# Optimization experiments

Hardware: AMD Instinct MI355X
Metric: run time of the kernel (lower is better)

The kernel has to match this reference:

```python
import jax, jax.numpy as jnp
import numpy as np

B, RNN, WV, VOCAB, SRC, NMEM, OOV = 64, 512, 512, 50000, 512, 512, 50


def _gru_cell(x, h, wih, whh, bih, bhh):
    # PyTorch GRU cell. x,h: (B,RNN); wih,whh: (3*RNN, RNN)
    gi = x @ wih.T + bih
    gh = h @ whh.T + bhh
    i_r, i_z, i_n = jnp.split(gi, 3, axis=-1)
    h_r, h_z, h_n = jnp.split(gh, 3, axis=-1)
    r = jax.nn.sigmoid(i_r + h_r)
    z = jax.nn.sigmoid(i_z + h_z)
    n = jnp.tanh(i_n + r * h_n)
    return (1.0 - z) * n + z * h


def _attn_general(q, K, V, mask, W):
    # q: (B,1,D), K/V: (B,N,D), mask: (B,N), W: (D,D) (torch Linear weight, out x in)
    e = jnp.einsum('bnd,ed->bne', K, W)          # W(K)
    e = e * mask[:, :, None]
    en = jnp.einsum('btd,bnd->btn', q, e)        # (B,1,N)
    en = en * mask[:, None, :]
    # masked softmax: exp * mask, renormalize
    m = mask[:, None, :]
    ex = jnp.exp(en - jnp.max(en, axis=-1, keepdims=True)) * m
    w = ex / (jnp.sum(ex, axis=-1, keepdims=True) + 1e-10)
    ctx = jnp.einsum('btn,bnd->btd', w, V)       # (B,1,D)
    return ctx, w, en


def setup_inputs() -> dict:
    key = jax.random.key(0)
    ks = jax.random.split(key, 24)
    s = 0.05
    inp = {
        'y_t_1': jax.random.randint(ks[0], (B,), 0, VOCAB),
        's_t_1': jax.random.normal(ks[1], (1, B, RNN)) * s,
        'encoder_outputs': jax.random.normal(ks[2], (B, SRC, RNN)) * s,
        'enc_padding_mask': jnp.ones((B, SRC), jnp.float32),
        'c_t_1': jax.random.normal(ks[3], (B, 1, RNN)) * s,
        'extra_zeros': jnp.zeros((B, OOV), jnp.float32),
        'enc_batch_extend_vocab': jax.random.randint(ks[4], (B, SRC), 0, VOCAB + OOV),
        'query_memory': jax.random.normal(ks[5], (B, NMEM, RNN)) * s,
        'query_mask': jnp.ones((B, NMEM), jnp.float32),
        # parameters
        'embedding': jax.random.normal(ks[6], (VOCAB, WV)) * s,
        'x_ctx_w': jax.random.normal(ks[7], (RNN, RNN + WV)) * s,
        'x_ctx_b': jnp.zeros((RNN,), jnp.float32),
        'gru_wih': jax.random.uniform(ks[8], (3 * RNN, RNN), minval=-0.1, maxval=0.1),
        'gru_whh': jax.random.uniform(ks[9], (3 * RNN, RNN), minval=-0.1, maxval=0.1),
        'gru_bih': jnp.concatenate([jnp.zeros(RNN), jnp.ones(RNN // 2), jnp.zeros(3 * RNN - RNN - RNN // 2)]).astype(jnp.float32),
        'gru_bhh': jnp.zeros((3 * RNN,), jnp.float32),
        'readq_w': jax.random.normal(ks[10], (RNN, RNN)) * s,
        'readsrc_w': jax.random.normal(ks[11], (RNN, RNN)) * s,
        'out1_w': jax.random.normal(ks[12], (RNN, 2 * RNN)) * s,
        'out1_b': jnp.zeros((RNN,), jnp.float32),
        'out2_w': jax.random.normal(ks[13], (VOCAB, RNN)) * s,
        'out2_b': jnp.zeros((VOCAB,), jnp.float32),
    }
    return inp


def reference(y_t_1, s_t_1, encoder_outputs, enc_padding_mask, c_t_1, extra_zeros,
              enc_batch_extend_vocab, query_memory, query_mask,
              embedding, x_ctx_w, x_ctx_b, gru_wih, gru_whh, gru_bih, gru_bhh,
              readq_w, readsrc_w, out1_w, out1_b, out2_w, out2_b):
    # embed current token and mix with previous context
    y_emb = embedding[y_t_1]                                   # (B,WV)
    x = jnp.concatenate([c_t_1, y_emb[:, None, :]], axis=-1)   # (B,1,RNN+WV)
    x = x @ x_ctx_w.T + x_ctx_b                                # (B,1,RNN)

    h = s_t_1[0]                                               # (B,RNN)
    h = _gru_cell(x[:, 0], h, gru_wih, gru_whh, gru_bih, gru_bhh)

    # NTM memory read + second GRU step (loop runs once in the source)
    c_mem, _, _ = _attn_general(h[:, None, :], query_memory, query_memory, query_mask, readq_w)
    h = _gru_cell(c_mem[:, 0], h, gru_wih, gru_whh, gru_bih, gru_bhh)

    # source attention
    c_t, attn_dist, _ = _attn_general(h[:, None, :], encoder_outputs, encoder_outputs, enc_padding_mask, readsrc_w)

    out = jnp.concatenate([h, c_t[:, 0]], axis=-1)             # (B,2*RNN)
    out = out @ out1_w.T + out1_b
    out = out @ out2_w.T + out2_b                              # (B,VOCAB)
    vocab_dist = jax.nn.softmax(out, axis=-1)

    vocab_dist_ = 0.5 * vocab_dist
    attn_dist_ = 0.5 * attn_dist[:, 0]                         # (B,SRC)
    vocab_dist_ = jnp.concatenate([vocab_dist_, extra_zeros], axis=-1)  # (B,VOCAB+OOV)

    # copy-mechanism scatter_add along vocab dim, per batch row
    final_dist = jax.vmap(lambda v, idx, a: v.at[idx].add(a))(
        vocab_dist_, enc_batch_extend_vocab, attn_dist_)

    s_t = h[None]                                              # (1,B,RNN)
    return final_dist, s_t, c_t, attn_dist
```

## Files before the change

### kernel.cpp

```cpp
#include <hip/hip_runtime.h>

#define BATCH 64
#define RNN   512
#define VOCAB 50000
#define OOV   50
#define VEXT  50050
#define NSRC  512

typedef short bf16x8 __attribute__((ext_vector_type(8)));
typedef float f32x4  __attribute__((ext_vector_type(4)));

__device__ __forceinline__ float sigmoidf_(float x) { return 1.f / (1.f + __expf(-x)); }

__device__ __forceinline__ short f2bf(float x) {
    unsigned u = __builtin_bit_cast(unsigned, x);
    unsigned r = (u + 0x7FFFu + ((u >> 16) & 1u)) >> 16;
    return (short)r;
}

__global__ void k_build_x0(const int* __restrict__ y, const float* __restrict__ c_t_1,
                           const float* __restrict__ emb, float* __restrict__ x0)
{
    const int b = blockIdx.x;
    const int row = y[b];
    for (int d = threadIdx.x; d < 512; d += 256) {
        x0[(size_t)b * 1024 + d]       = c_t_1[(size_t)b * 512 + d];
        x0[(size_t)b * 1024 + 512 + d] = emb[(size_t)row * 512 + d];
    }
}

template<bool WT>
__global__ __launch_bounds__(256) void k_gemm_small(
    const float* __restrict__ A0, const float* __restrict__ W0,
    const float* __restrict__ bias0, float* __restrict__ C0, int asum0,
    const float* __restrict__ A1, const float* __restrict__ W1,
    const float* __restrict__ bias1, float* __restrict__ C1, int asum1,
    int K, int O)
{
    const float* A = A0; const float* W = W0; const float* bias = bias0;
    float* C = C0; int asum = asum0;
    if (blockIdx.z == 1) { A = A1; W = W1; bias = bias1; C = C1; asum = asum1; }

    __shared__ float As[32 * 64];
    __shared__ float Ws[32 * 32];
    const int t  = threadIdx.x;
    const int tx = t & 15, ty = t >> 4;
    const int o0 = blockIdx.x * 32;
    const int kchunk = K >> 2;
    const int kbeg = blockIdx.y * kchunk;
    const int kend = kbeg + kchunk;
    float acc[4][2] = {};
    const int ab  = t >> 2;
    const int akq = (t & 3) * 4;

    for (int k0 = kbeg; k0 < kend; k0 += 32) {
        {
            const float* Ap = &A[(size_t)ab * K + k0 + akq];
            float4 v0 = *(const float4*)Ap;
            float4 v1 = *(const float4*)(Ap + 16);
            if (asum) {
                #pragma unroll
                for (int s = 1; s < 4; s++) {
                    const float* Aps = Ap + (size_t)s * 64 * K;
                    float4 w0 = *(const float4*)Aps;
                    float4 w1 = *(const float4*)(Aps + 16);
                    v0.x += w0.x; v0.y += w0.y; v0.z += w0.z; v0.w += w0.w;
                    v1.x += w1.x; v1.y += w1.y; v1.z += w1.z; v1.w += w1.w;
                }
            }
            As[(akq+0)*64+ab]=v0.x; As[(akq+1)*64+ab]=v0.y; As[(akq+2)*64+ab]=v0.z; As[(akq+3)*64+ab]=v0.w;
            As[(akq+16)*64+ab]=v1.x; As[(akq+17)*64+ab]=v1.y; As[(akq+18)*64+ab]=v1.z; As[(akq+19)*64+ab]=v1.w;
        }
        if (WT) {
            const int o  = t >> 3;
            const int kq = (t & 7) * 4;
            float4 v = *(const float4*)&W[(size_t)(o0 + o) * K + k0 + kq];
            Ws[(kq+0)*32+o]=v.x; Ws[(kq+1)*32+o]=v.y; Ws[(kq+2)*32+o]=v.z; Ws[(kq+3)*32+o]=v.w;
        } else {
            const int kk = t >> 3;
            const int oq = (t & 7) * 4;
            *(float4*)&Ws[kk*32 + oq] = *(const float4*)&W[(size_t)(k0 + kk) * O + o0 + oq];
        }
        __syncthreads();
        #pragma unroll
        for (int kk = 0; kk < 32; kk++) {
            float4 a4 = *(const float4*)&As[kk*64 + ty*4];
            float2 w2 = *(const float2*)&Ws[kk*32 + tx*2];
            acc[0][0] = fmaf(a4.x, w2.x, acc[0][0]); acc[0][1] = fmaf(a4.x, w2.y, acc[0][1]);
            acc[1][0] = fmaf(a4.y, w2.x, acc[1][0]); acc[1][1] = fmaf(a4.y, w2.y, acc[1][1]);
            acc[2][0] = fmaf(a4.z, w2.x, acc[2][0]); acc[2][1] = fmaf(a4.z, w2.y, acc[2][1]);
            acc[3][0] = fmaf(a4.w, w2.x, acc[3][0]); acc[3][1] = fmaf(a4.w, w2.y, acc[3][1]);
        }
        __syncthreads();
    }
    const int o = o0 + tx*2;
    float b0v = 0.f, b1v = 0.f;
    if (bias && blockIdx.y == 0) { b0v = bias[o]; b1v = bias[o+1]; }
    float* Cp = C + (size_t)blockIdx.y * 64 * O;
    #pragma unroll
    for (int j = 0; j < 4; j++) {
        const int bb = ty*4 + j;
        Cp[(size_t)bb*O + o]     = acc[j][0] + b0v;
        Cp[(size_t)bb*O + o + 1] = acc[j][1] + b1v;
    }
}

__global__ void k_gru_elem(const float* __restrict__ gi, const float* __restrict__ gh,
                           const float* __restrict__ h, float* __restrict__ hout,
                           float* __restrict__ cat_out)
{
    const int b = blockIdx.x, d = threadIdx.x;
    float ir = 0, iz = 0, inn = 0, hr = 0, hz = 0, hn = 0;
    #pragma unroll
    for (int s = 0; s < 4; s++) {
        const float* gis = gi + (size_t)s * BATCH * 1536 + (size_t)b * 1536;
        const float* ghs = gh + (size_t)s * BATCH * 1536 + (size_t)b * 1536;
        ir += gis[d]; iz += gis[512 + d]; inn += gis[1024 + d];
        hr += ghs[d]; hz += ghs[512 + d]; hn += ghs[1024 + d];
    }
    const float r = sigmoidf_(ir + hr);
    const float z = sigmoidf_(iz + hz);
    const float n = tanhf(inn + r * hn);
    const float hv = (1.f - z) * n + z * h[(size_t)b * 512 + d];
    hout[(size_t)b * 512 + d] = hv;
    if (cat_out) cat_out[(size_t)b * 1024 + d] = hv;
}

__global__ __launch_bounds__(256) void k_attn_pass(
    const float* __restrict__ KV, const float* __restrict__ Upart,
    const float* __restrict__ mask, float* __restrict__ en, float* __restrict__ part)
{
    const int b = blockIdx.y;
    const int chunk = blockIdx.x;
    const int t = threadIdx.x;
    const int lane = t & 63;
    const int wv = t >> 6;
    const float* KVb = KV + (size_t)b * NSRC * RNN;

    const int r0 = chunk * 32 + wv * 8;

    float4 x[8][2];
    float mk[8];
    #pragma unroll
    for (int i = 0; i < 8; i++) {
        const float* rp = KVb + (size_t)(r0 + i) * RNN + lane * 8;
        x[i][0] = *(const float4*)rp;
        x[i][1] = *(const float4*)(rp + 4);
    }
    #pragma unroll
    for (int i = 0; i < 8; i++) mk[i] = mask[(size_t)b * NSRC + r0 + i];

    float4 u0, u1;
    {
        const float* up = Upart + (size_t)b * RNN + lane * 8;
        u0 = *(const float4*)up; u1 = *(const float4*)(up + 4);
        #pragma unroll
        for (int s = 1; s < 4; s++) {
            const float* ups = up + (size_t)s * BATCH * RNN;
            float4 a = *(const float4*)ups; float4 c = *(const float4*)(ups + 4);
            u0.x += a.x; u0.y += a.y; u0.z += a.z; u0.w += a.w;
            u1.x += c.x; u1.y += c.y; u1.z += c.z; u1.w += c.w;
        }
    }

    float m_run = -1e30f, s_run = 0.f;
    float acc[8] = {0,0,0,0,0,0,0,0};
    #pragma unroll
    for (int i = 0; i < 8; i++) {
        const int n = r0 + i;
        float d = x[i][0].x*u0.x + x[i][0].y*u0.y + x[i][0].z*u0.z + x[i][0].w*u0.w
                + x[i][1].x*u1.x + x[i][1].y*u1.y + x[i][1].z*u1.z + x[i][1].w*u1.w;
        #pragma unroll
        for (int off = 32; off; off >>= 1) d += __shfl_xor(d, off);
        const float s = d * mk[i] * mk[i];
        if (lane == 0) en[(size_t)b * NSRC + n] = s;
        const float mnew = fmaxf(m_run, s);
        const float sc = __expf(m_run - mnew);
        const float w  = __expf(s - mnew) * mk[i];
        s_run = s_run * sc + w;
        acc[0] = acc[0]*sc + w*x[i][0].x; acc[1] = acc[1]*sc + w*x[i][0].y;
        acc[2] = acc[2]*sc + w*x[i][0].z; acc[3] = acc[3]*sc + w*x[i][0].w;
        acc[4] = acc[4]*sc + w*x[i][1].x; acc[5] = acc[5]*sc + w*x[i][1].y;
        acc[6] = acc[6]*sc + w*x[i][1].z; acc[7] = acc[7]*sc + w*x[i][1].w;
        m_run = mnew;
    }
    __shared__ float sm[4], ss[4];
    __shared__ float sacc[4][512];
    *(float4*)&sacc[wv][lane*8]     = make_float4(acc[0], acc[1], acc[2], acc[3]);
    *(float4*)&sacc[wv][lane*8 + 4] = make_float4(acc[4], acc[5], acc[6], acc[7]);
    if (lane == 0) { sm[wv] = m_run; ss[wv] = s_run; }
    __syncthreads();
    const float M = fmaxf(fmaxf(sm[0], sm[1]), fmaxf(sm[2], sm[3]));
    const float e0 = __expf(sm[0]-M), e1 = __expf(sm[1]-M), e2 = __expf(sm[2]-M), e3 = __expf(sm[3]-M);
    const float S = ss[0]*e0 + ss[1]*e1 + ss[2]*e2 + ss[3]*e3;
    float* pp = part + (size_t)(b * 16 + chunk) * 514;
    const int c = t;
    pp[2 + c]       = sacc[0][c]*e0 + sacc[1][c]*e1 + sacc[2][c]*e2 + sacc[3][c]*e3;
    pp[2 + c + 256] = sacc[0][c+256]*e0 + sacc[1][c+256]*e1 + sacc[2][c+256]*e2 + sacc[3][c+256]*e3;
    if (t == 0) { pp[0] = M; pp[1] = S; }
}

__global__ __launch_bounds__(256) void k_attn_combine(
    const float* __restrict__ part, const float* __restrict__ en,
    const float* __restrict__ mask, float* __restrict__ ctx,
    float* __restrict__ ctx2, float* __restrict__ attn_out)
{
    const int b = blockIdx.x, t = threadIdx.x;
    const float* pb = part + (size_t)b * 16 * 514;
    float M = -1e30f;
    #pragma unroll
    for (int c = 0; c < 16; c++) M = fmaxf(M, pb[c * 514]);
    float e[16]; float S = 0.f;
    #pragma unroll
    for (int c = 0; c < 16; c++) { e[c] = __expf(pb[c * 514] - M); S += pb[c * 514 + 1] * e[c]; }
    const float inv = 1.f / (S + 1e-10f);
    for (int d = t; d < 512; d += 256) {
        float a = 0.f;
        #pragma unroll
        for (int c = 0; c < 16; c++) a += pb[c * 514 + 2 + d] * e[c];
        const float val = a * inv;
        ctx[(size_t)b * 512 + d] = val;
        if (ctx2) ctx2[(size_t)b * 1024 + d] = val;
    }
    if (attn_out) {
        for (int n = t; n < NSRC; n += 256)
            attn_out[(size_t)b * NSRC + n] = __expf(en[(size_t)b * NSRC + n] - M) * mask[(size_t)b * NSRC + n] * inv;
    }
}

__global__ void k_tobf16(const float* __restrict__ in, short* __restrict__ outp)
{
    const int i = blockIdx.x * 256 + threadIdx.x;
    const float v = in[i] + in[32768 + i] + in[65536 + i] + in[98304 + i];
    outp[i] = f2bf(v);
}

__global__ __launch_bounds__(512, 4) void k_out2_mfma(
    const short* __restrict__ Abf, const float* __restrict__ W2,
    const float* __restrict__ bias, float* __restrict__ C)
{
    __shared__ alignas(16) short As[64 * 512];
    const int t = threadIdx.x;
    const int lane = t & 63, wv = t >> 6;

    {
        char* Asb = (char*)As;
        const char* Ab = (const char*)Abf;
        #pragma unroll
        for (int it = 0; it < 8; ++it) {
            const int off = (it * 512 + t) * 16;
            const int row = off >> 10;
            const int kb  = off & 1023;
            bf16x8 v = *(const bf16x8*)(Ab + off);
            *(bf16x8*)(Asb + row * 1024 + (kb ^ ((row & 7) << 4))) = v;
        }
    }
    __syncthreads();

    const int l15 = lane & 15, g = lane >> 4;
    const int goff = g * 8;
    const int obase = blockIdx.x * 128 + wv * 16;
    const int ocol = obase + l15;
    const int orow = (ocol < VOCAB) ? ocol : (VOCAB - 1);
    const float* wr = &W2[(size_t)orow * RNN + goff];

    const int sw = (l15 & 7) << 4;
    const char* a0b = (const char*)As + (l15     ) * 1024;
    const char* a1b = (const char*)As + (l15 + 16) * 1024;
    const char* a2b = (const char*)As + (l15 + 32) * 1024;
    const char* a3b = (const char*)As + (l15 + 48) * 1024;

    f32x4 acc0 = {0,0,0,0}, acc1 = {0,0,0,0}, acc2 = {0,0,0,0}, acc3 = {0,0,0,0};

    float4 p0a = *(const float4*)(wr);
    float4 p0b = *(const float4*)(wr + 4);
    float4 p1a = *(const float4*)(wr + 32);
    float4 p1b = *(const float4*)(wr + 36);
    #pragma unroll 4
    for (int k0 = 0; k0 < RNN; k0 += 32) {
        const int kn = (k0 + 64) & 511;
        float4 n0 = *(const float4*)(wr + kn);
        float4 n1 = *(const float4*)(wr + kn + 4);
        const int kb = ((k0 + goff) * 2) ^ sw;
        bf16x8 a0 = *(const bf16x8*)(a0b + kb);
        bf16x8 a1 = *(const bf16x8*)(a1b + kb);
        bf16x8 a2 = *(const bf16x8*)(a2b + kb);
        bf16x8 a3 = *(const bf16x8*)(a3b + kb);
        bf16x8 bf;
        bf[0]=f2bf(p0a.x); bf[1]=f2bf(p0a.y); bf[2]=f2bf(p0a.z); bf[3]=f2bf(p0a.w);
        bf[4]=f2bf(p0b.x); bf[5]=f2bf(p0b.y); bf[6]=f2bf(p0b.z); bf[7]=f2bf(p0b.w);
        acc0 = __builtin_amdgcn_mfma_f32_16x16x32_bf16(a0, bf, acc0, 0, 0, 0);
        acc1 = __builtin_amdgcn_mfma_f32_16x16x32_bf16(a1, bf, acc1, 0, 0, 0);
        acc2 = __builtin_amdgcn_mfma_f32_16x16x32_bf16(a2, bf, acc2, 0, 0, 0);
        acc3 = __builtin_amdgcn_mfma_f32_16x16x32_bf16(a3, bf, acc3, 0, 0, 0);
        p0a = p1a; p0b = p1b; p1a = n0; p1b = n1;
    }
    if (ocol < VOCAB) {
        const float bv = bias[ocol];
        #pragma unroll
        for (int r = 0; r < 4; r++) {
            C[(size_t)(     g*4 + r) * VOCAB + ocol] = acc0[r] + bv;
            C[(size_t)(16 + g*4 + r) * VOCAB + ocol] = acc1[r] + bv;
            C[(size_t)(32 + g*4 + r) * VOCAB + ocol] = acc2[r] + bv;
            C[(size_t)(48 + g*4 + r) * VOCAB + ocol] = acc3[r] + bv;
        }
    }
}

__global__ __launch_bounds__(256) void k_rowstat(const float* __restrict__ L, float* __restrict__ stat)
{
    const int b = blockIdx.x, t = threadIdx.x;
    const float* row = L + (size_t)b * VOCAB;
    __shared__ float red[4];
    float m = -1e30f;
    for (int v = t * 4; v < VOCAB; v += 1024) {
        float4 x = *(const float4*)&row[v];
        m = fmaxf(m, fmaxf(fmaxf(x.x, x.y), fmaxf(x.z, x.w)));
    }
    #pragma unroll
    for (int off = 32; off; off >>= 1) m = fmaxf(m, __shfl_xor(m, off));
    if ((t & 63) == 0) red[t >> 6] = m;
    __syncthreads();
    m = fmaxf(fmaxf(red[0], red[1]), fmaxf(red[2], red[3]));
    __syncthreads();
    float s = 0.f;
    for (int v = t * 4; v < VOCAB; v += 1024) {
        float4 x = *(const float4*)&row[v];
        s += __expf(x.x - m) + __expf(x.y - m) + __expf(x.z - m) + __expf(x.w - m);
    }
    #pragma unroll
    for (int off = 32; off; off >>= 1) s += __shfl_xor(s, off);
    if ((t & 63) == 0) red[t >> 6] = s;
    __syncthreads();
    s = red[0] + red[1] + red[2] + red[3];
    if (t == 0) { stat[b * 2] = m; stat[b * 2 + 1] = s; }
}

__global__ void k_final(const float* __restrict__ L, const float* __restrict__ stat,
                        const float* __restrict__ ez, float* __restrict__ out)
{
    const int b = blockIdx.y;
    const int v = blockIdx.x * 256 + threadIdx.x;
    if (v >= VEXT) return;
    const float M = stat[b * 2];
    const float inv = 0.5f / stat[b * 2 + 1];
    float r;
    if (v < VOCAB) r = __expf(L[(size_t)b * VOCAB + v] - M) * inv;
    else           r = ez[(size_t)b * OOV + (v - VOCAB)];
    out[(size_t)b * VEXT + v] = r;
}

__global__ void k_scatter(const int* __restrict__ idx, const float* __restrict__ attn,
                          float* __restrict__ out)
{
    const int b = blockIdx.x, j = threadIdx.x;
    const int v = idx[(size_t)b * NSRC + j];
    atomicAdd(&out[(size_t)b * VEXT + v], 0.5f * attn[(size_t)b * NSRC + j]);
}

extern "C" void kernel_launch(void* const* d_in, const int* in_sizes, int n_in,
                              void* d_out, int out_size, void* d_ws, size_t ws_size,
                              hipStream_t stream)
{
    (void)in_sizes; (void)n_in; (void)out_size; (void)ws_size;
    const int*   y     = (const int*)  d_in[0];
    const float* st1   = (const float*)d_in[1];
    const float* enc   = (const float*)d_in[2];
    const float* encM  = (const float*)d_in[3];
    const float* ct1   = (const float*)d_in[4];
    const float* ez    = (const float*)d_in[5];
    const int*   ebev  = (const int*)  d_in[6];
    const float* qmem  = (const float*)d_in[7];
    const float* qmask = (const float*)d_in[8];
    const float* emb   = (const float*)d_in[9];
    const float* xw    = (const float*)d_in[10];
    const float* xb    = (const float*)d_in[11];
    const float* wih   = (const float*)d_in[12];
    const float* whh   = (const float*)d_in[13];
    const float* bih   = (const float*)d_in[14];
    const float* bhh   = (const float*)d_in[15];
    const float* rqw   = (const float*)d_in[16];
    const float* rsw   = (const float*)d_in[17];
    const float* o1w   = (const float*)d_in[18];
    const float* o1b   = (const float*)d_in[19];
    const float* o2w   = (const float*)d_in[20];
    const float* o2b   = (const float*)d_in[21];

    float* ws  = (float*)d_ws;
    float* out = (float*)d_out;

    constexpr size_t WS_X0   = 0;
    constexpr size_t WS_PART = 65536;
    constexpr size_t WS_EN   = 591872;
    constexpr size_t WS_H1   = 624640;
    constexpr size_t WS_CTX1 = 657408;
    constexpr size_t WS_LOG  = 0;
    constexpr size_t WS_XP   = 3200000;
    constexpr size_t WS_GIP  = 3331072;
    constexpr size_t WS_GHP  = 3724288;
    constexpr size_t WS_UP   = 4117504;
    constexpr size_t WS_O1P  = 4248576;
    constexpr size_t WS_CAT2 = 4379648;
    constexpr size_t WS_STAT = 4445184;
    constexpr size_t WS_ABF  = 4445312;

    constexpr size_t OUT_ST = 3203200, OUT_CT = 3235968, OUT_ATTN = 3268736;

    float* x0   = ws + WS_X0;
    float* part = ws + WS_PART;
    float* en   = ws + WS_EN;
    float* h1   = ws + WS_H1;
    float* ctx1 = ws + WS_CTX1;
    float* logi = ws + WS_LOG;
    float* xp   = ws + WS_XP;
    float* gip  = ws + WS_GIP;
    float* ghp  = ws + WS_GHP;
    float* up   = ws + WS_UP;
    float* o1p  = ws + WS_O1P;
    float* cat2 = ws + WS_CAT2;
    float* stat = ws + WS_STAT;
    short* abf  = (short*)(ws + WS_ABF);

    k_build_x0<<<64, 256, 0, stream>>>(y, ct1, emb, x0);
    k_gemm_small<true><<<dim3(16,4,1), 256, 0, stream>>>(x0, xw, xb, xp, 0,
                                                         nullptr, nullptr, nullptr, nullptr, 0, 1024, 512);
    k_gemm_small<true><<<dim3(48,4,2), 256, 0, stream>>>(xp, wih, bih, gip, 1,
                                                         st1, whh, bhh, ghp, 0, 512, 1536);
    k_gru_elem<<<64, 512, 0, stream>>>(gip, ghp, st1, h1, nullptr);
    k_gemm_small<false><<<dim3(16,4,1), 256, 0, stream>>>(h1, rqw, nullptr, up, 0,
                                                          nullptr, nullptr, nullptr, nullptr, 0, 512, 512);
    k_attn_pass<<<dim3(16,64), 256, 0, stream>>>(qmem, up, qmask, en, part);
    k_attn_combine<<<64, 256, 0, stream>>>(part, en, qmask, ctx1, nullptr, nullptr);
    k_gemm_small<true><<<dim3(48,4,2), 256, 0, stream>>>(ctx1, wih, bih, gip, 0,
                                                         h1, whh, bhh, ghp, 0, 512, 1536);
    k_gru_elem<<<64, 512, 0, stream>>>(gip, ghp, h1, out + OUT_ST, cat2);
    k_gemm_small<false><<<dim3(16,4,1), 256, 0, stream>>>(out + OUT_ST, rsw, nullptr, up, 0,
                                                          nullptr, nullptr, nullptr, nullptr, 0, 512, 512);
    k_attn_pass<<<dim3(16,64), 256, 0, stream>>>(enc, up, encM, en, part);
    k_attn_combine<<<64, 256, 0, stream>>>(part, en, encM, out + OUT_CT, cat2 + 512, out + OUT_ATTN);
    k_gemm_small<true><<<dim3(16,4,1), 256, 0, stream>>>(cat2, o1w, o1b, o1p, 0,
                                                         nullptr, nullptr, nullptr, nullptr, 0, 1024, 512);
    k_tobf16<<<128, 256, 0, stream>>>(o1p, abf);
    k_out2_mfma<<<391, 512, 0, stream>>>(abf, o2w, o2b, logi);
    k_rowstat<<<64, 256, 0, stream>>>(logi, stat);
    k_final<<<dim3(196,64), 256, 0, stream>>>(logi, stat, ez, out);
    k_scatter<<<64, 512, 0, stream>>>(ebev, out + OUT_ATTN, out);
}
```

Baseline: 164.6 us.

## Fuse GRU elementwise into query GEMMs, embedding gather into x GEMM, softmax stats into vocab GEMM

Folds the embedding gather into the first projection GEMM and folds the GRU elementwise step into the prologue of the following query-projection GEMM, which now uses split-K 8. It also computes per-block softmax max and sum partials in the epilogue of the vocab MFMA GEMM, so a small reduction kernel replaces the full 64x50000 logit rescan. The combine kernel gets a wider grid. The goal is fewer launches and less global memory traffic, at the cost of recomputing GRU values in each column block.

```diff
diff --git a/kernel.cpp b/kernel.cpp
--- a/kernel.cpp
+++ b/kernel.cpp
@@ -6,27 +6,26 @@
 #define OOV   50
 #define VEXT  50050
 #define NSRC  512
+#define NOB2  391
 
 typedef short bf16x8 __attribute__((ext_vector_type(8)));
 typedef float f32x4  __attribute__((ext_vector_type(4)));
 
 __device__ __forceinline__ float sigmoidf_(float x) { return 1.f / (1.f + __expf(-x)); }
+
+__device__ __forceinline__ float gru_one(float ir, float iz, float inn,
+                                         float hr, float hz, float hn, float h)
+{
+    const float r = sigmoidf_(ir + hr);
+    const float z = sigmoidf_(iz + hz);
+    const float n = tanhf(inn + r * hn);
+    return (1.f - z) * n + z * h;
+}
 
 __device__ __forceinline__ short f2bf(float x) {
     unsigned u = __builtin_bit_cast(unsigned, x);
     unsigned r = (u + 0x7FFFu + ((u >> 16) & 1u)) >> 16;
     return (short)r;
-}
-
-__global__ void k_build_x0(const int* __restrict__ y, const float* __restrict__ c_t_1,
-                           const float* __restrict__ emb, float* __restrict__ x0)
-{
-    const int b = blockIdx.x;
-    const int row = y[b];
-    for (int d = threadIdx.x; d < 512; d += 256) {
-        x0[(size_t)b * 1024 + d]       = c_t_1[(size_t)b * 512 + d];
-        x0[(size_t)b * 1024 + 512 + d] = emb[(size_t)row * 512 + d];
-    }
 }
 
 template<bool WT>
@@ -105,25 +104,141 @@
     }
 }
 
-__global__ void k_gru_elem(const float* __restrict__ gi, const float* __restrict__ gh,
-                           const float* __restrict__ h, float* __restrict__ hout,
-                           float* __restrict__ cat_out)
-{
-    const int b = blockIdx.x, d = threadIdx.x;
-    float ir = 0, iz = 0, inn = 0, hr = 0, hz = 0, hn = 0;
-    #pragma unroll
-    for (int s = 0; s < 4; s++) {
-        const float* gis = gi + (size_t)s * BATCH * 1536 + (size_t)b * 1536;
-        const float* ghs = gh + (size_t)s * BATCH * 1536 + (size_t)b * 1536;
-        ir += gis[d]; iz += gis[512 + d]; inn += gis[1024 + d];
-        hr += ghs[d]; hz += ghs[512 + d]; hn += ghs[1024 + d];
-    }
-    const float r = sigmoidf_(ir + hr);
-    const float z = sigmoidf_(iz + hz);
-    const float n = tanhf(inn + r * hn);
-    const float hv = (1.f - z) * n + z * h[(size_t)b * 512 + d];
-    hout[(size_t)b * 512 + d] = hv;
-    if (cat_out) cat_out[(size_t)b * 1024 + d] = hv;
+__global__ __launch_bounds__(256) void k_gemm_x0(
+    const int* __restrict__ yidx, const float* __restrict__ ct1, const float* __restrict__ emb,
+    const float* __restrict__ W, const float* __restrict__ bias, float* __restrict__ C)
+{
+    __shared__ float As[32 * 64];
+    __shared__ float Ws[32 * 32];
+    const int t  = threadIdx.x;
+    const int tx = t & 15, ty = t >> 4;
+    const int o0 = blockIdx.x * 32;
+    const int kbeg = blockIdx.y * 256;
+    const int kend = kbeg + 256;
+    float acc[4][2] = {};
+    const int ab  = t >> 2;
+    const int akq = (t & 3) * 4;
+    const int erow = yidx[ab];
+
+    for (int k0 = kbeg; k0 < kend; k0 += 32) {
+        {
+            const float* src = (k0 < 512) ? (ct1 + (size_t)ab * 512 + k0)
+                                          : (emb + (size_t)erow * 512 + (k0 - 512));
+            float4 v0 = *(const float4*)(src + akq);
+            float4 v1 = *(const float4*)(src + akq + 16);
+            As[(akq+0)*64+ab]=v0.x; As[(akq+1)*64+ab]=v0.y; As[(akq+2)*64+ab]=v0.z; As[(akq+3)*64+ab]=v0.w;
+            As[(akq+16)*64+ab]=v1.x; As[(akq+17)*64+ab]=v1.y; As[(akq+18)*64+ab]=v1.z; As[(akq+19)*64+ab]=v1.w;
+        }
+        {
+            const int o  = t >> 3;
+            const int kq = (t & 7) * 4;
+            float4 v = *(const float4*)&W[(size_t)(o0 + o) * 1024 + k0 + kq];
+            Ws[(kq+0)*32+o]=v.x; Ws[(kq+1)*32+o]=v.y; Ws[(kq+2)*32+o]=v.z; Ws[(kq+3)*32+o]=v.w;
+        }
+        __syncthreads();
+        #pragma unroll
+        for (int kk = 0; kk < 32; kk++) {
+            float4 a4 = *(const float4*)&As[kk*64 + ty*4];
+            float2 w2 = *(const float2*)&Ws[kk*32 + tx*2];
+            acc[0][0] = fmaf(a4.x, w2.x, acc[0][0]); acc[0][1] = fmaf(a4.x, w2.y, acc[0][1]);
+            acc[1][0] = fmaf(a4.y, w2.x, acc[1][0]); acc[1][1] = fmaf(a4.y, w2.y, acc[1][1]);
+            acc[2][0] = fmaf(a4.z, w2.x, acc[2][0]); acc[2][1] = fmaf(a4.z, w2.y, acc[2][1]);
+            acc[3][0] = fmaf(a4.w, w2.x, acc[3][0]); acc[3][1] = fmaf(a4.w, w2.y, acc[3][1]);
+        }
+        __syncthreads();
+    }
+    const int o = o0 + tx*2;
+    float b0v = 0.f, b1v = 0.f;
+    if (blockIdx.y == 0) { b0v = bias[o]; b1v = bias[o+1]; }
+    float* Cp = C + (size_t)blockIdx.y * 64 * 512;
+    #pragma unroll
+    for (int j = 0; j < 4; j++) {
+        const int bb = ty*4 + j;
+        Cp[(size_t)bb*512 + o]     = acc[j][0] + b0v;
+        Cp[(size_t)bb*512 + o + 1] = acc[j][1] + b1v;
+    }
+}
+
+template<int KS>
+__global__ __launch_bounds__(256) void k_gemm_gru(
+    const float* __restrict__ gi, const float* __restrict__ gh,
+    const float* __restrict__ hprev, const float* __restrict__ W,
+    float* __restrict__ C, float* __restrict__ hout, float* __restrict__ cat_out)
+{
+    __shared__ float As[32 * 64];
+    __shared__ float Ws[32 * 32];
+    const int t  = threadIdx.x;
+    const int tx = t & 15, ty = t >> 4;
+    const int o0 = blockIdx.x * 32;
+    const int kchunk = 512 / KS;
+    const int kbeg = blockIdx.y * kchunk;
+    const int kend = kbeg + kchunk;
+    float acc[4][2] = {};
+    const int ab  = t >> 2;
+    const int akq = (t & 3) * 4;
+
+    for (int k0 = kbeg; k0 < kend; k0 += 32) {
+        #pragma unroll
+        for (int half = 0; half < 2; half++) {
+            const int d = k0 + akq + half * 16;
+            float irv[4] = {0,0,0,0}, izv[4] = {0,0,0,0}, inv_[4] = {0,0,0,0};
+            float hrv[4] = {0,0,0,0}, hzv[4] = {0,0,0,0}, hnv[4] = {0,0,0,0};
+            #pragma unroll
+            for (int s = 0; s < 4; s++) {
+                const float* gp = gi + (size_t)s * BATCH * 1536 + (size_t)ab * 1536 + d;
+                const float* hp = gh + (size_t)s * BATCH * 1536 + (size_t)ab * 1536 + d;
+                float4 a0 = *(const float4*)(gp);
+                float4 a1 = *(const float4*)(gp + 512);
+                float4 a2 = *(const float4*)(gp + 1024);
+                float4 b0 = *(const float4*)(hp);
+                float4 b1 = *(const float4*)(hp + 512);
+                float4 b2 = *(const float4*)(hp + 1024);
+                irv[0]+=a0.x; irv[1]+=a0.y; irv[2]+=a0.z; irv[3]+=a0.w;
+                izv[0]+=a1.x; izv[1]+=a1.y; izv[2]+=a1.z; izv[3]+=a1.w;
+                inv_[0]+=a2.x; inv_[1]+=a2.y; inv_[2]+=a2.z; inv_[3]+=a2.w;
+                hrv[0]+=b0.x; hrv[1]+=b0.y; hrv[2]+=b0.z; hrv[3]+=b0.w;
+                hzv[0]+=b1.x; hzv[1]+=b1.y; hzv[2]+=b1.z; hzv[3]+=b1.w;
+                hnv[0]+=b2.x; hnv[1]+=b2.y; hnv[2]+=b2.z; hnv[3]+=b2.w;
+            }
+            const float4 hq = *(const float4*)(hprev + (size_t)ab * 512 + d);
+            float o0v = gru_one(irv[0], izv[0], inv_[0], hrv[0], hzv[0], hnv[0], hq.x);
+            float o1v = gru_one(irv[1], izv[1], inv_[1], hrv[1], hzv[1], hnv[1], hq.y);
+            float o2v = gru_one(irv[2], izv[2], inv_[2], hrv[2], hzv[2], hnv[2], hq.z);
+            float o3v = gru_one(irv[3], izv[3], inv_[3], hrv[3], hzv[3], hnv[3], hq.w);
+            const int kk = akq + half * 16;
+            As[(kk+0)*64+ab] = o0v; As[(kk+1)*64+ab] = o1v;
+            As[(kk+2)*64+ab] = o2v; As[(kk+3)*64+ab] = o3v;
+            if (blockIdx.x == 0) {
+                float4 ov = make_float4(o0v, o1v, o2v, o3v);
+                *(float4*)&hout[(size_t)ab * 512 + d] = ov;
+                if (cat_out) *(float4*)&cat_out[(size_t)ab * 1024 + d] = ov;
+            }
+        }
+        {
+            const int kk = t >> 3;
+            const int oq = (t & 7) * 4;
+            *(float4*)&Ws[kk*32 + oq] = *(const float4*)&W[(size_t)(k0 + kk) * 512 + o0 + oq];
+        }
+        __syncthreads();
+        #pragma unroll
+        for (int kk = 0; kk < 32; kk++) {
+            float4 a4 = *(const float4*)&As[kk*64 + ty*4];
+            float2 w2 = *(const float2*)&Ws[kk*32 + tx*2];
+            acc[0][0] = fmaf(a4.x, w2.x, acc[0][0]); acc[0][1] = fmaf(a4.x, w2.y, acc[0][1]);
+            acc[1][0] = fmaf(a4.y, w2.x, acc[1][0]); acc[1][1] = fmaf(a4.y, w2.y, acc[1][1]);
+            acc[2][0] = fmaf(a4.z, w2.x, acc[2][0]); acc[2][1] = fmaf(a4.z, w2.y, acc[2][1]);
+            acc[3][0] = fmaf(a4.w, w2.x, acc[3][0]); acc[3][1] = fmaf(a4.w, w2.y, acc[3][1]);
+        }
+        __syncthreads();
+    }
+    const int o = o0 + tx*2;
+    float* Cp = C + (size_t)blockIdx.y * 64 * 512;
+    #pragma unroll
+    for (int j = 0; j < 4; j++) {
+        const int bb = ty*4 + j;
+        Cp[(size_t)bb*512 + o]     = acc[j][0];
+        Cp[(size_t)bb*512 + o + 1] = acc[j][1];
+    }
 }
 
 __global__ __launch_bounds__(256) void k_attn_pass(
@@ -155,7 +270,7 @@
         const float* up = Upart + (size_t)b * RNN + lane * 8;
         u0 = *(const float4*)up; u1 = *(const float4*)(up + 4);
         #pragma unroll
-        for (int s = 1; s < 4; s++) {
+        for (int s = 1; s < 8; s++) {
             const float* ups = up + (size_t)s * BATCH * RNN;
             float4 a = *(const float4*)ups; float4 c = *(const float4*)(ups + 4);
             u0.x += a.x; u0.y += a.y; u0.z += a.z; u0.w += a.w;
@@ -200,12 +315,12 @@
     if (t == 0) { pp[0] = M; pp[1] = S; }
 }
 
-__global__ __launch_bounds__(256) void k_attn_combine(
+__global__ __launch_bounds__(128) void k_attn_combine(
     const float* __restrict__ part, const float* __restrict__ en,
     const float* __restrict__ mask, float* __restrict__ ctx,
     float* __restrict__ ctx2, float* __restrict__ attn_out)
 {
-    const int b = blockIdx.x, t = threadIdx.x;
+    const int b = blockIdx.x, z = blockIdx.y, t = threadIdx.x;
     const float* pb = part + (size_t)b * 16 * 514;
     float M = -1e30f;
     #pragma unroll
@@ -214,18 +329,15 @@
     #pragma unroll
     for (int c = 0; c < 16; c++) { e[c] = __expf(pb[c * 514] - M); S += pb[c * 514 + 1] * e[c]; }
     const float inv = 1.f / (S + 1e-10f);
-    for (int d = t; d < 512; d += 256) {
-        float a = 0.f;
-        #pragma unroll
-        for (int c = 0; c < 16; c++) a += pb[c * 514 + 2 + d] * e[c];
-        const float val = a * inv;
-        ctx[(size_t)b * 512 + d] = val;
-        if (ctx2) ctx2[(size_t)b * 1024 + d] = val;
-    }
-    if (attn_out) {
-        for (int n = t; n < NSRC; n += 256)
-            attn_out[(size_t)b * NSRC + n] = __expf(en[(size_t)b * NSRC + n] - M) * mask[(size_t)b * NSRC + n] * inv;
-    }
+    const int d = z * 128 + t;
+    float a = 0.f;
+    #pragma unroll
+    for (int c = 0; c < 16; c++) a += pb[c * 514 + 2 + d] * e[c];
+    const float val = a * inv;
+    ctx[(size_t)b * 512 + d] = val;
+    if (ctx2) ctx2[(size_t)b * 1024 + d] = val;
+    if (attn_out)
+        attn_out[(size_t)b * NSRC + d] = __expf(en[(size_t)b * NSRC + d] - M) * mask[(size_t)b * NSRC + d] * inv;
 }
 
 __global__ void k_tobf16(const float* __restrict__ in, short* __restrict__ outp)
@@ -237,9 +349,11 @@
 
 __global__ __launch_bounds__(512, 4) void k_out2_mfma(
     const short* __restrict__ Abf, const float* __restrict__ W2,
-    const float* __restrict__ bias, float* __restrict__ C)
+    const float* __restrict__ bias, float* __restrict__ C, float* __restrict__ bstat)
 {
     __shared__ alignas(16) short As[64 * 512];
+    __shared__ float smax[8][64];
+    __shared__ float ssum[8][64];
     const int t = threadIdx.x;
     const int lane = t & 63, wv = t >> 6;
 
@@ -261,7 +375,8 @@
     const int goff = g * 8;
     const int obase = blockIdx.x * 128 + wv * 16;
     const int ocol = obase + l15;
-    const int orow = (ocol < VOCAB) ? ocol : (VOCAB - 1);
+    const bool valid = (ocol < VOCAB);
+    const int orow = valid ? ocol : (VOCAB - 1);
     const float* wr = &W2[(size_t)orow * RNN + goff];
 
     const int sw = (l15 & 7) << 4;
@@ -295,28 +410,74 @@
         acc3 = __builtin_amdgcn_mfma_f32_16x16x32_bf16(a3, bf, acc3, 0, 0, 0);
         p0a = p1a; p0b = p1b; p1a = n0; p1b = n1;
     }
-    if (ocol < VOCAB) {
-        const float bv = bias[ocol];
+
+    const float bv = valid ? bias[ocol] : 0.f;
+    float lv[4][4];
+    #pragma unroll
+    for (int r = 0; r < 4; r++) {
+        lv[0][r] = valid ? acc0[r] + bv : -1e30f;
+        lv[1][r] = valid ? acc1[r] + bv : -1e30f;
+        lv[2][r] = valid ? acc2[r] + bv : -1e30f;
+        lv[3][r] = valid ? acc3[r] + bv : -1e30f;
+    }
+    if (valid) {
+        #pragma unroll
+        for (int q = 0; q < 4; q++)
+            #pragma unroll
+            for (int r = 0; r < 4; r++)
+                C[(size_t)(q*16 + g*4 + r) * VOCAB + ocol] = lv[q][r];
+    }
+
+    #pragma unroll
+    for (int q = 0; q < 4; q++) {
         #pragma unroll
         for (int r = 0; r < 4; r++) {
-            C[(size_t)(     g*4 + r) * VOCAB + ocol] = acc0[r] + bv;
-            C[(size_t)(16 + g*4 + r) * VOCAB + ocol] = acc1[r] + bv;
-            C[(size_t)(32 + g*4 + r) * VOCAB + ocol] = acc2[r] + bv;
-            C[(size_t)(48 + g*4 + r) * VOCAB + ocol] = acc3[r] + bv;
-        }
-    }
-}
-
-__global__ __launch_bounds__(256) void k_rowstat(const float* __restrict__ L, float* __restrict__ stat)
+            float m = lv[q][r];
+            m = fmaxf(m, __shfl_xor(m, 1));
+            m = fmaxf(m, __shfl_xor(m, 2));
+            m = fmaxf(m, __shfl_xor(m, 4));
+            m = fmaxf(m, __shfl_xor(m, 8));
+            if (l15 == 0) smax[wv][q*16 + g*4 + r] = m;
+        }
+    }
+    __syncthreads();
+    if (t < 64) {
+        float m = smax[0][t];
+        #pragma unroll
+        for (int w = 1; w < 8; w++) m = fmaxf(m, smax[w][t]);
+        smax[0][t] = m;
+    }
+    __syncthreads();
+    #pragma unroll
+    for (int q = 0; q < 4; q++) {
+        #pragma unroll
+        for (int r = 0; r < 4; r++) {
+            const int row = q*16 + g*4 + r;
+            float e = __expf(lv[q][r] - smax[0][row]);
+            e += __shfl_xor(e, 1);
+            e += __shfl_xor(e, 2);
+            e += __shfl_xor(e, 4);
+            e += __shfl_xor(e, 8);
+            if (l15 == 0) ssum[wv][row] = e;
+        }
+    }
+    __syncthreads();
+    if (t < 64) {
+        float s = 0.f;
+        #pragma unroll
+        for (int w = 0; w < 8; w++) s += ssum[w][t];
+        bstat[((size_t)t * NOB2 + blockIdx.x) * 2 + 0] = smax[0][t];
+        bstat[((size_t)t * NOB2 + blockIdx.x) * 2 + 1] = s;
+    }
+}
+
+__global__ __launch_bounds__(256) void k_statred(const float* __restrict__ bstat, float* __restrict__ stat)
 {
     const int b = blockIdx.x, t = threadIdx.x;
-    const float* row = L + (size_t)b * VOCAB;
-    __shared__ float red[4];
+    const float* pr = bstat + (size_t)b * NOB2 * 2;
+    __shared__ float red[8];
     float m = -1e30f;
-    for (int v = t * 4; v < VOCAB; v += 1024) {
-        float4 x = *(const float4*)&row[v];
-        m = fmaxf(m, fmaxf(fmaxf(x.x, x.y), fmaxf(x.z, x.w)));
-    }
+    for (int i = t; i < NOB2; i += 256) m = fmaxf(m, pr[i*2]);
     #pragma unroll
     for (int off = 32; off; off >>= 1) m = fmaxf(m, __shfl_xor(m, off));
     if ((t & 63) == 0) red[t >> 6] = m;
@@ -324,16 +485,12 @@
     m = fmaxf(fmaxf(red[0], red[1]), fmaxf(red[2], red[3]));
     __syncthreads();
     float s = 0.f;
-    for (int v = t * 4; v < VOCAB; v += 1024) {
-        float4 x = *(const float4*)&row[v];
-        s += __expf(x.x - m) + __expf(x.y - m) + __expf(x.z - m) + __expf(x.w - m);
-    }
+    for (int i = t; i < NOB2; i += 256) s += pr[i*2+1] * __expf(pr[i*2] - m);
     #pragma unroll
     for (int off = 32; off; off >>= 1) s += __shfl_xor(s, off);
-    if ((t & 63) == 0) red[t >> 6] = s;
-    __syncthreads();
-    s = red[0] + red[1] + red[2] + red[3];
-    if (t == 0) { stat[b * 2] = m; stat[b * 2 + 1] = s; }
+    if ((t & 63) == 0) red[(t >> 6) + 4] = s;
+    __syncthreads();
+    if (t == 0) { stat[b*2] = m; stat[b*2+1] = red[4]+red[5]+red[6]+red[7]; }
 }
 
 __global__ void k_final(const float* __restrict__ L, const float* __restrict__ stat,
@@ -389,60 +546,54 @@
     float* ws  = (float*)d_ws;
     float* out = (float*)d_out;
 
-    constexpr size_t WS_X0   = 0;
-    constexpr size_t WS_PART = 65536;
-    constexpr size_t WS_EN   = 591872;
-    constexpr size_t WS_H1   = 624640;
-    constexpr size_t WS_CTX1 = 657408;
+    constexpr size_t WS_PART = 0;
+    constexpr size_t WS_EN   = 526336;
+    constexpr size_t WS_H1   = 559104;
+    constexpr size_t WS_CTX1 = 591872;
     constexpr size_t WS_LOG  = 0;
-    constexpr size_t WS_XP   = 3200000;
-    constexpr size_t WS_GIP  = 3331072;
-    constexpr size_t WS_GHP  = 3724288;
-    constexpr size_t WS_UP   = 4117504;
-    constexpr size_t WS_O1P  = 4248576;
-    constexpr size_t WS_CAT2 = 4379648;
-    constexpr size_t WS_STAT = 4445184;
-    constexpr size_t WS_ABF  = 4445312;
+    constexpr size_t WS_GIP  = 3200000;
+    constexpr size_t WS_GHP  = 3593216;
+    constexpr size_t WS_UP   = 3986432;
+    constexpr size_t WS_XP   = 3986432;
+    constexpr size_t WS_O1P  = 3986432;
+    constexpr size_t WS_ABF  = 4117504;
+    constexpr size_t WS_CAT2 = 4248576;
+    constexpr size_t WS_BSTAT= 4314112;
+    constexpr size_t WS_STAT = 4364160;
 
     constexpr size_t OUT_ST = 3203200, OUT_CT = 3235968, OUT_ATTN = 3268736;
 
-    float* x0   = ws + WS_X0;
     float* part = ws + WS_PART;
     float* en   = ws + WS_EN;
     float* h1   = ws + WS_H1;
     float* ctx1 = ws + WS_CTX1;
     float* logi = ws + WS_LOG;
-    float* xp   = ws + WS_XP;
     float* gip  = ws + WS_GIP;
     float* ghp  = ws + WS_GHP;
     float* up   = ws + WS_UP;
+    float* xp   = ws + WS_XP;
     float* o1p  = ws + WS_O1P;
     float* cat2 = ws + WS_CAT2;
+    float* bstat= ws + WS_BSTAT;
     float* stat = ws + WS_STAT;
     short* abf  = (short*)(ws + WS_ABF);
 
-    k_build_x0<<<64, 256, 0, stream>>>(y, ct1, emb, x0);
-    k_gemm_small<true><<<dim3(16,4,1), 256, 0, stream>>>(x0, xw, xb, xp, 0,
-                                                         nullptr, nullptr, nullptr, nullptr, 0, 1024, 512);
+    k_gemm_x0<<<dim3(16,4), 256, 0, stream>>>(y, ct1, emb, xw, xb, xp);
     k_gemm_small<true><<<dim3(48,4,2), 256, 0, stream>>>(xp, wih, bih, gip, 1,
                                                          st1, whh, bhh, ghp, 0, 512, 1536);
-    k_gru_elem<<<64, 512, 0, stream>>>(gip, ghp, st1, h1, nullptr);
-    k_gemm_small<false><<<dim3(16,4,1), 256, 0, stream>>>(h1, rqw, nullptr, up, 0,
-                                                          nullptr, nullptr, nullptr, nullptr, 0, 512, 512);
+    k_gemm_gru<8><<<dim3(16,8), 256, 0, stream>>>(gip, ghp, st1, rqw, up, h1, nullptr);
     k_attn_pass<<<dim3(16,64), 256, 0, stream>>>(qmem, up, qmask, en, part);
-    k_attn_combine<<<64, 256, 0, stream>>>(part, en, qmask, ctx1, nullptr, nullptr);
+    k_attn_combine<<<dim3(64,4), 128, 0, stream>>>(part, en, qmask, ctx1, nullptr, nullptr);
     k_gemm_small<true><<<dim3(48,4,2), 256, 0, stream>>>(ctx1, wih, bih, gip, 0,
                                                          h1, whh, bhh, ghp, 0, 512, 1536);
-    k_gru_elem<<<64, 512, 0, stream>>>(gip, ghp, h1, out + OUT_ST, cat2);
-    k_gemm_small<false><<<dim3(16,4,1), 256, 0, stream>>>(out + OUT_ST, rsw, nullptr, up, 0,
-                                                          nullptr, nullptr, nullptr, nullptr, 0, 512, 512);
+    k_gemm_gru<8><<<dim3(16,8), 256, 0, stream>>>(gip, ghp, h1, rsw, up, out + OUT_ST, cat2);
     k_attn_pass<<<dim3(16,64), 256, 0, stream>>>(enc, up, encM, en, part);
-    k_attn_combine<<<64, 256, 0, stream>>>(part, en, encM, out + OUT_CT, cat2 + 512, out + OUT_ATTN);
+    k_attn_combine<<<dim3(64,4), 128, 0, stream>>>(part, en, encM, out + OUT_CT, cat2 + 512, out + OUT_ATTN);
     k_gemm_small<true><<<dim3(16,4,1), 256, 0, stream>>>(cat2, o1w, o1b, o1p, 0,
                                                          nullptr, nullptr, nullptr, nullptr, 0, 1024, 512);
     k_tobf16<<<128, 256, 0, stream>>>(o1p, abf);
-    k_out2_mfma<<<391, 512, 0, stream>>>(abf, o2w, o2b, logi);
-    k_rowstat<<<64, 256, 0, stream>>>(logi, stat);
+    k_out2_mfma<<<NOB2, 512, 0, stream>>>(abf, o2w, o2b, logi, bstat);
+    k_statred<<<64, 256, 0, stream>>>(bstat, stat);
     k_final<<<dim3(196,64), 256, 0, stream>>>(logi, stat, ez, out);
     k_scatter<<<64, 512, 0, stream>>>(ebev, out + OUT_ATTN, out);
 }
```

New measurement: 156.8 us. 1.05x faster.
